# Optimization experiments

Hardware: AMD Instinct MI355X
Metric: run time of the kernel (lower is better)

Reference implementation:

```python
import jax, jax.numpy as jnp
import numpy as np

TOP_K = 2
CAP_FACTOR = 1.25


def _gelu(x):
    # custom tanh GELU matching the torch module
    return 0.5 * x * (1.0 + jnp.tanh(jnp.sqrt(2.0 / jnp.pi) * (x + 0.044715 * x ** 3)))


def setup_inputs() -> dict:
    key = jax.random.key(0)
    ks = jax.random.split(key, 6)
    B, S, D, F, E = 4, 2048, 1024, 4096, 8
    return {
        "hidden_states": jax.random.normal(ks[0], (B, S, D), dtype=jnp.float32),
        "wr": jax.random.normal(ks[1], (E, D), dtype=jnp.float32) * 0.02,  # router weight (Linear, no bias)
        "w1": jax.random.normal(ks[2], (E, D, F), dtype=jnp.float32) * 0.02,
        "b1": jnp.zeros((E, F), dtype=jnp.float32),
        "w2": jax.random.normal(ks[3], (E, F, D), dtype=jnp.float32) * 0.02,
        "b2": jnp.zeros((E, D), dtype=jnp.float32),
    }


def reference(hidden_states, wr, w1, b1, w2, b2):
    B, S, D = hidden_states.shape
    E = wr.shape[0]
    x = hidden_states.reshape(-1, D)  # [T, D]
    T = x.shape[0]

    # ---- router (eval mode: no noise) ----
    logits = x @ wr.T  # [T, E]
    vals, idx = jax.lax.top_k(logits, TOP_K)  # [T, K]
    sparse = jnp.full((T, E), -jnp.inf, dtype=logits.dtype)
    sparse = sparse.at[jnp.arange(T)[:, None], idx].set(vals)
    gating = jax.nn.softmax(sparse, axis=-1)  # [T, E], zero off top-k

    # ---- capacity-limited dispatch ----
    cap = max(8, int(max(1, T * TOP_K // E) * CAP_FACTOR))
    mask = (idx[:, :, None] == jnp.arange(E)).any(axis=1)  # [T, E]
    pos = jnp.cumsum(mask.astype(jnp.int32), axis=0) - 1  # rank of token within expert
    keep = mask & (pos < cap)
    slot = jnp.where(keep, pos, cap)  # overflow -> dummy slot
    e_grid = jnp.broadcast_to(jnp.arange(E)[None, :], (T, E))
    t_grid = jnp.broadcast_to(jnp.arange(T)[:, None], (T, E))
    dispatch = jnp.full((E, cap + 1), T, dtype=jnp.int32)
    dispatch = dispatch.at[e_grid, slot].set(t_grid)[:, :cap]  # [E, cap], T = pad

    # ---- grouped expert MLP ----
    x_pad = jnp.concatenate([x, jnp.zeros((1, D), x.dtype)], axis=0)
    g_pad = jnp.concatenate([gating, jnp.zeros((1, E), gating.dtype)], axis=0)
    xg = x_pad[dispatch]  # [E, cap, D]
    h = _gelu(jnp.einsum('ecd,edf->ecf', xg, w1) + b1[:, None, :])
    y = jnp.einsum('ecf,efd->ecd', h, w2) + b2[:, None, :]  # [E, cap, D]
    g = g_pad[dispatch, jnp.arange(E)[:, None]]  # [E, cap]; 0 for padded slots
    wy = y * g[..., None]

    # ---- combine (scatter-add) ----
    out = jax.ops.segment_sum(wy.reshape(-1, D), dispatch.reshape(-1), num_segments=T + 1)[:T]
    return out.reshape(B, S, D)
```

## Files before the change

kernel.cpp:

```cpp
#include <hip/hip_runtime.h>
#include <cstdint>
#include <cstddef>

#define T_TOK 8192
#define D_DIM 1024
#define F_DIM 4096
#define E_NUM 8
#define CAP   2560
#define BKS   32
#define MYB   20

typedef __attribute__((ext_vector_type(8))) short bf16x8;
typedef __attribute__((ext_vector_type(4))) float f32x4;

typedef const __attribute__((address_space(1))) void* gas_ptr;
typedef __attribute__((address_space(3))) void* las_ptr;

__device__ __forceinline__ unsigned short f2bf(float f) {
  unsigned u = __float_as_uint(f);
  u += 0x7FFF + ((u >> 16) & 1);
  return (unsigned short)(u >> 16);
}

__device__ __forceinline__ float gelu_f(float x) {
  float u = 0.7978845608028654f * (x + 0.044715f * x * x * x);
  float t = 1.0f - 2.0f / (__expf(2.0f * u) + 1.0f);
  return 0.5f * x * (1.0f + t);
}

__device__ __forceinline__ int xcd_swizzle(int bid, int nwg) {
  int q = nwg >> 3;
  return (bid & 7) * q + (bid >> 3);
}

__global__ __launch_bounds__(256) void route_kernel(
    const float* __restrict__ x, const float* __restrict__ wr,
    unsigned short* __restrict__ xbf, int2* __restrict__ tokE,
    float2* __restrict__ tokG)
{
  int tid = threadIdx.x;
  int l = tid & 63;
  int w = tid >> 6;
  int t = blockIdx.x * 4 + w;
  const float4* xr = (const float4*)(x + (size_t)t * D_DIM);
  ushort4* xbr = (ushort4*)(xbf + (size_t)t * D_DIM);
  float acc[E_NUM];
#pragma unroll
  for (int e = 0; e < E_NUM; ++e) acc[e] = 0.f;
#pragma unroll
  for (int c = 0; c < D_DIM / 256; ++c) {
    float4 xv = xr[c * 64 + l];
    ushort4 bv;
    bv.x = f2bf(xv.x); bv.y = f2bf(xv.y); bv.z = f2bf(xv.z); bv.w = f2bf(xv.w);
    xbr[c * 64 + l] = bv;
#pragma unroll
    for (int e = 0; e < E_NUM; ++e) {
      float4 wv = ((const float4*)(wr + (size_t)e * D_DIM))[c * 64 + l];
      acc[e] += xv.x * wv.x + xv.y * wv.y + xv.z * wv.z + xv.w * wv.w;
    }
  }
#pragma unroll
  for (int e = 0; e < E_NUM; ++e) {
#pragma unroll
    for (int s = 32; s > 0; s >>= 1) acc[e] += __shfl_xor(acc[e], s);
  }
  if (l == 0) {
    int e1 = 0; float v1 = acc[0];
#pragma unroll
    for (int e = 1; e < E_NUM; ++e) if (acc[e] > v1) { v1 = acc[e]; e1 = e; }
    int e2 = -1; float v2 = -3.4e38f;
#pragma unroll
    for (int e = 0; e < E_NUM; ++e) if (e != e1 && acc[e] > v2) { v2 = acc[e]; e2 = e; }
    float s = __expf(v2 - v1);
    float g1 = 1.f / (1.f + s);
    tokE[t] = make_int2(e1, e2);
    tokG[t] = make_float2(g1, s * g1);
  }
}

__global__ __launch_bounds__(256) void scan_kernel(
    const int2* __restrict__ tokE, const float2* __restrict__ tokG,
    int* __restrict__ dispatch, float* __restrict__ sgate)
{
  int e = blockIdx.x;
  int tid = threadIdx.x;
  int l = tid & 63;
  int w = tid >> 6;
  __shared__ int wsum[4];
  int base = 0;
  for (int chunk = 0; chunk < T_TOK; chunk += 256) {
    int t = chunk + tid;
    int2 te = tokE[t];
    float2 tg = tokG[t];
    bool f1 = (te.x == e);
    bool f2 = (te.y == e);
    bool f = f1 || f2;
    unsigned long long m = __ballot(f);
    int rank = __popcll(m & ((1ull << l) - 1ull));
    if (l == 0) wsum[w] = __popcll(m);
    __syncthreads();
    int woff = 0;
#pragma unroll
    for (int i = 0; i < 4; ++i) if (i < w) woff += wsum[i];
    int tot = wsum[0] + wsum[1] + wsum[2] + wsum[3];
    int pos = base + woff + rank;
    if (f && pos < CAP) {
      dispatch[e * CAP + pos] = t;
      sgate[e * CAP + pos] = f1 ? tg.x : tg.y;
    }
    base += tot;
    __syncthreads();
  }
  int start = base < CAP ? base : CAP;
  for (int p = start + tid; p < CAP; p += 256) {
    dispatch[e * CAP + p] = T_TOK;
    sgate[e * CAP + p] = 0.f;
  }
}

__global__ __launch_bounds__(256) void transpose_kernel(
    const float* __restrict__ src, unsigned short* __restrict__ dst,
    int K, int N)
{
  const float* s = src + (size_t)blockIdx.z * K * N;
  unsigned short* d = dst + (size_t)blockIdx.z * K * N;
  __shared__ float tile[32][33];
  int tx = threadIdx.x & 31;
  int ty = threadIdx.x >> 5;
  int n0 = blockIdx.x * 32;
  int k0 = blockIdx.y * 32;
#pragma unroll
  for (int i = 0; i < 4; ++i)
    tile[ty + i * 8][tx] = s[(size_t)(k0 + ty + i * 8) * N + n0 + tx];
  __syncthreads();
#pragma unroll
  for (int i = 0; i < 4; ++i)
    d[(size_t)(n0 + ty + i * 8) * K + k0 + tx] = f2bf(tile[tx][ty + i * 8]);
}

#define G1_NXB (F_DIM / 128)
__global__ __launch_bounds__(256, 4) void gemm1_kernel(
    const unsigned short* __restrict__ xbf,
    const unsigned short* __restrict__ w1t,
    const float* __restrict__ b1,
    const int* __restrict__ dispatch,
    unsigned short* __restrict__ h,
    int e_base, size_t w1stride, size_t hstride)
{
  int wg = xcd_swizzle(blockIdx.x, gridDim.x);
  int my = wg % MYB;
  int p  = wg / MYB;
  int nx = p % G1_NXB;
  int ez = p / G1_NXB;
  int e = e_base + ez;
  const unsigned short* w1e = w1t + (size_t)ez * w1stride;
  unsigned short* he = h + (size_t)ez * hstride;
  int n0 = nx * 128;
  int m0 = my * 128;
  int tid = threadIdx.x;
  int l = tid & 63;
  int wid = tid >> 6;
  int wm = wid >> 1, wn = wid & 1;
  int lrow = l & 15, lhi = l >> 4;

  __shared__ __align__(16) unsigned short As[2][128 * BKS];
  __shared__ __align__(16) unsigned short Bs[2][128 * BKS];

  int slot = tid & 3;
  const unsigned short* asrc[2];
  const unsigned short* bsrc[2];
#pragma unroll
  for (int i = 0; i < 2; ++i) {
    int row = i * 64 + (tid >> 2);
    int r = m0 + row;
    int tok = (r < CAP) ? dispatch[e * CAP + r] : T_TOK;
    asrc[i] = xbf + (size_t)tok * D_DIM + slot * 8;
    bsrc[i] = w1e + (size_t)(n0 + row) * D_DIM + slot * 8;
  }

  f32x4 acc[4][4];
#pragma unroll
  for (int m = 0; m < 4; ++m)
#pragma unroll
    for (int n = 0; n < 4; ++n) acc[m][n] = (f32x4){0.f, 0.f, 0.f, 0.f};

  const int NK = D_DIM / BKS;
#pragma unroll
  for (int i = 0; i < 2; ++i) {
    __builtin_amdgcn_global_load_lds((gas_ptr)(asrc[i]),
        (las_ptr)&As[0][(i * 256 + wid * 64) * 8], 16, 0, 0);
    __builtin_amdgcn_global_load_lds((gas_ptr)(bsrc[i]),
        (las_ptr)&Bs[0][(i * 256 + wid * 64) * 8], 16, 0, 0);
  }
  __syncthreads();

  for (int t = 0; t < NK; ++t) {
    int cur = t & 1;
    if (t + 1 < NK) {
      int nxt = cur ^ 1;
      int k0 = (t + 1) * BKS;
#pragma unroll
      for (int i = 0; i < 2; ++i) {
        __builtin_amdgcn_global_load_lds((gas_ptr)(asrc[i] + k0),
            (las_ptr)&As[nxt][(i * 256 + wid * 64) * 8], 16, 0, 0);
        __builtin_amdgcn_global_load_lds((gas_ptr)(bsrc[i] + k0),
            (las_ptr)&Bs[nxt][(i * 256 + wid * 64) * 8], 16, 0, 0);
      }
    }
    bf16x8 af[4], bfr[4];
#pragma unroll
    for (int m = 0; m < 4; ++m) {
      int row = wm * 64 + m * 16 + lrow;
      af[m] = *(const bf16x8*)&As[cur][row * BKS + lhi * 8];
    }
#pragma unroll
    for (int n = 0; n < 4; ++n) {
      int col = wn * 64 + n * 16 + lrow;
      bfr[n] = *(const bf16x8*)&Bs[cur][col * BKS + lhi * 8];
    }
#pragma unroll
    for (int m = 0; m < 4; ++m)
#pragma unroll
      for (int n = 0; n < 4; ++n)
        acc[m][n] = __builtin_amdgcn_mfma_f32_16x16x32_bf16(af[m], bfr[n], acc[m][n], 0, 0, 0);
    __syncthreads();
  }

  int colg[4]; float b1v[4];
#pragma unroll
  for (int n = 0; n < 4; ++n) {
    colg[n] = n0 + wn * 64 + n * 16 + lrow;
    b1v[n] = b1[e * F_DIM + colg[n]];
  }
#pragma unroll
  for (int m = 0; m < 4; ++m) {
    int rb = m0 + wm * 64 + m * 16 + lhi * 4;
#pragma unroll
    for (int j = 0; j < 4; ++j) {
      int r = rb + j;
      if (r < CAP) {
        unsigned short* hr = he + (size_t)r * F_DIM;
#pragma unroll
        for (int n = 0; n < 4; ++n) {
          float v = acc[m][n][j] + b1v[n];
          hr[colg[n]] = f2bf(gelu_f(v));
        }
      }
    }
  }
}

#define G2_NXB (D_DIM / 128)
__global__ __launch_bounds__(256, 4) void gemm2_kernel(
    const unsigned short* __restrict__ h,
    const unsigned short* __restrict__ w2t,
    const float* __restrict__ b2,
    const int* __restrict__ dispatch,
    const float* __restrict__ sgate,
    float* __restrict__ out,
    int e_base, size_t w2stride, size_t hstride)
{
  int wg = xcd_swizzle(blockIdx.x, gridDim.x);
  int my = wg % MYB;
  int p  = wg / MYB;
  int nx = p % G2_NXB;
  int ez = p / G2_NXB;
  int e = e_base + ez;
  const unsigned short* he = h + (size_t)ez * hstride;
  const unsigned short* w2e = w2t + (size_t)ez * w2stride;
  int n0 = nx * 128;
  int m0 = my * 128;
  int tid = threadIdx.x;
  int l = tid & 63;
  int wid = tid >> 6;
  int wm = wid >> 1, wn = wid & 1;
  int lrow = l & 15, lhi = l >> 4;

  __shared__ __align__(16) unsigned short As[2][128 * BKS];
  __shared__ __align__(16) unsigned short Bs[2][128 * BKS];

  int slot = tid & 3;
  const unsigned short* asrc[2];
  const unsigned short* bsrc[2];
#pragma unroll
  for (int i = 0; i < 2; ++i) {
    int row = i * 64 + (tid >> 2);
    int r = m0 + row; if (r >= CAP) r = CAP - 1;
    asrc[i] = he + (size_t)r * F_DIM + slot * 8;
    bsrc[i] = w2e + (size_t)(n0 + row) * F_DIM + slot * 8;
  }

  f32x4 acc[4][4];
#pragma unroll
  for (int m = 0; m < 4; ++m)
#pragma unroll
    for (int n = 0; n < 4; ++n) acc[m][n] = (f32x4){0.f, 0.f, 0.f, 0.f};

  const int NK = F_DIM / BKS;
#pragma unroll
  for (int i = 0; i < 2; ++i) {
    __builtin_amdgcn_global_load_lds((gas_ptr)(asrc[i]),
        (las_ptr)&As[0][(i * 256 + wid * 64) * 8], 16, 0, 0);
    __builtin_amdgcn_global_load_lds((gas_ptr)(bsrc[i]),
        (las_ptr)&Bs[0][(i * 256 + wid * 64) * 8], 16, 0, 0);
  }
  __syncthreads();

  for (int t = 0; t < NK; ++t) {
    int cur = t & 1;
    if (t + 1 < NK) {
      int nxt = cur ^ 1;
      int k0 = (t + 1) * BKS;
#pragma unroll
      for (int i = 0; i < 2; ++i) {
        __builtin_amdgcn_global_load_lds((gas_ptr)(asrc[i] + k0),
            (las_ptr)&As[nxt][(i * 256 + wid * 64) * 8], 16, 0, 0);
        __builtin_amdgcn_global_load_lds((gas_ptr)(bsrc[i] + k0),
            (las_ptr)&Bs[nxt][(i * 256 + wid * 64) * 8], 16, 0, 0);
      }
    }
    bf16x8 af[4], bfr[4];
#pragma unroll
    for (int m = 0; m < 4; ++m) {
      int row = wm * 64 + m * 16 + lrow;
      af[m] = *(const bf16x8*)&As[cur][row * BKS + lhi * 8];
    }
#pragma unroll
    for (int n = 0; n < 4; ++n) {
      int col = wn * 64 + n * 16 + lrow;
      bfr[n] = *(const bf16x8*)&Bs[cur][col * BKS + lhi * 8];
    }
#pragma unroll
    for (int m = 0; m < 4; ++m)
#pragma unroll
      for (int n = 0; n < 4; ++n)
        acc[m][n] = __builtin_amdgcn_mfma_f32_16x16x32_bf16(af[m], bfr[n], acc[m][n], 0, 0, 0);
    __syncthreads();
  }

  int colg[4]; float b2v[4];
#pragma unroll
  for (int n = 0; n < 4; ++n) {
    colg[n] = n0 + wn * 64 + n * 16 + lrow;
    b2v[n] = b2[e * D_DIM + colg[n]];
  }
#pragma unroll
  for (int m = 0; m < 4; ++m) {
    int rb = m0 + wm * 64 + m * 16 + lhi * 4;
#pragma unroll
    for (int j = 0; j < 4; ++j) {
      int r = rb + j;
      if (r < CAP) {
        int tok = dispatch[e * CAP + r];
        if (tok < T_TOK) {
          float g = sgate[e * CAP + r];
          float* orow = out + (size_t)tok * D_DIM;
#pragma unroll
          for (int n = 0; n < 4; ++n)
            atomicAdd(&orow[colg[n]], g * (acc[m][n][j] + b2v[n]));
        }
      }
    }
  }
}

extern "C" void kernel_launch(void* const* d_in, const int* in_sizes, int n_in,
                              void* d_out, int out_size, void* d_ws, size_t ws_size,
                              hipStream_t stream) {
  const float* x  = (const float*)d_in[0];
  const float* wr = (const float*)d_in[1];
  const float* w1 = (const float*)d_in[2];
  const float* b1 = (const float*)d_in[3];
  const float* w2 = (const float*)d_in[4];
  const float* b2 = (const float*)d_in[5];
  float* out = (float*)d_out;

  char* ws = (char*)d_ws;
  size_t off = 0;
  auto alloc = [&](size_t bytes) -> void* {
    off = (off + 255) & ~(size_t)255;
    void* p = ws + off;
    off += bytes;
    return p;
  };
  int*   dispatch = (int*)alloc((size_t)E_NUM * CAP * 4);
  float* sgate    = (float*)alloc((size_t)E_NUM * CAP * 4);
  int2*  tokE     = (int2*)alloc((size_t)T_TOK * 8);
  float2* tokG    = (float2*)alloc((size_t)T_TOK * 8);
  unsigned short* xbf = (unsigned short*)alloc((size_t)(T_TOK + 1) * D_DIM * 2);

  const size_t wsz = (size_t)D_DIM * F_DIM * 2;
  const size_t hsz = (size_t)CAP * F_DIM * 2;
  size_t remain = ws_size > off ? ws_size - off : 0;
  bool tierA = remain >= (size_t)E_NUM * (2 * wsz + hsz) + (size_t)(1 << 16);

  hipMemsetAsync(out, 0, (size_t)T_TOK * D_DIM * 4, stream);
  hipMemsetAsync(xbf + (size_t)T_TOK * D_DIM, 0, D_DIM * 2, stream);
  route_kernel<<<T_TOK / 4, 256, 0, stream>>>(x, wr, xbf, tokE, tokG);
  scan_kernel<<<E_NUM, 256, 0, stream>>>(tokE, tokG, dispatch, sgate);

  if (tierA) {
    unsigned short* w1t = (unsigned short*)alloc((size_t)E_NUM * wsz);
    unsigned short* w2t = (unsigned short*)alloc((size_t)E_NUM * wsz);
    unsigned short* hb  = (unsigned short*)alloc((size_t)E_NUM * hsz);
    transpose_kernel<<<dim3(F_DIM / 32, D_DIM / 32, E_NUM), 256, 0, stream>>>(w1, w1t, D_DIM, F_DIM);
    transpose_kernel<<<dim3(D_DIM / 32, F_DIM / 32, E_NUM), 256, 0, stream>>>(w2, w2t, F_DIM, D_DIM);
    gemm1_kernel<<<dim3(G1_NXB * MYB * E_NUM), 256, 0, stream>>>(
        xbf, w1t, b1, dispatch, hb, 0, wsz / 2, hsz / 2);
    gemm2_kernel<<<dim3(G2_NXB * MYB * E_NUM), 256, 0, stream>>>(
        hb, w2t, b2, dispatch, sgate, out, 0, wsz / 2, hsz / 2);
  } else {
    unsigned short* w1t = (unsigned short*)alloc(wsz);
    unsigned short* w2t = (unsigned short*)alloc(wsz);
    unsigned short* hb  = (unsigned short*)alloc(hsz);
    for (int e = 0; e < E_NUM; ++e) {
      transpose_kernel<<<dim3(F_DIM / 32, D_DIM / 32, 1), 256, 0, stream>>>(
          w1 + (size_t)e * D_DIM * F_DIM, w1t, D_DIM, F_DIM);
      gemm1_kernel<<<dim3(G1_NXB * MYB), 256, 0, stream>>>(
          xbf, w1t, b1, dispatch, hb, e, 0, 0);
      transpose_kernel<<<dim3(D_DIM / 32, F_DIM / 32, 1), 256, 0, stream>>>(
          w2 + (size_t)e * D_DIM * F_DIM, w2t, F_DIM, D_DIM);
      gemm2_kernel<<<dim3(G2_NXB * MYB), 256, 0, stream>>>(
          hb, w2t, b2, dispatch, sgate, out, e, 0, 0);
    }
  }
}
```

Measured before the change: 874.0 us.

## Triple-buffer swizzled GEMM pipeline, skip empty expert tiles, vectorize weight transpose

Both expert GEMMs move from a double-buffered loop with full __syncthreads to a three-stage LDS ring. It waits with vmcnt-based barriers, uses XOR-swizzled LDS layouts to avoid bank conflicts, and raises MFMA priority. The scan kernel now records per-expert token counts, so GEMM blocks whose row tile lies beyond an expert's filled capacity exit early. The weight transpose uses 64x64 tiles with float4 loads and 16-byte bf16 stores. The added LDS per block lowers the occupancy hint from 4 to 3 blocks per CU, and early exit depends on routing balance.

```diff
diff --git a/kernel.cpp b/kernel.cpp
--- a/kernel.cpp
+++ b/kernel.cpp
@@ -9,8 +9,10 @@
 #define CAP   2560
 #define BKS   32
 #define MYB   20
+#define LDSB  16384
 
 typedef __attribute__((ext_vector_type(8))) short bf16x8;
+typedef __attribute__((ext_vector_type(8))) unsigned short u16x8;
 typedef __attribute__((ext_vector_type(4))) float f32x4;
 
 typedef const __attribute__((address_space(1))) void* gas_ptr;
@@ -32,6 +34,9 @@
   int q = nwg >> 3;
   return (bid & 7) * q + (bid >> 3);
 }
+
+#define PIPE_BAR4() asm volatile("s_waitcnt vmcnt(4)\n\ts_barrier" ::: "memory")
+#define PIPE_BAR0() asm volatile("s_waitcnt vmcnt(0)\n\ts_barrier" ::: "memory")
 
 __global__ __launch_bounds__(256) void route_kernel(
     const float* __restrict__ x, const float* __restrict__ wr,
@@ -80,7 +85,7 @@
 
 __global__ __launch_bounds__(256) void scan_kernel(
     const int2* __restrict__ tokE, const float2* __restrict__ tokG,
-    int* __restrict__ dispatch, float* __restrict__ sgate)
+    int* __restrict__ dispatch, float* __restrict__ sgate, int* __restrict__ cnt)
 {
   int e = blockIdx.x;
   int tid = threadIdx.x;
@@ -116,6 +121,7 @@
     dispatch[e * CAP + p] = T_TOK;
     sgate[e * CAP + p] = 0.f;
   }
+  if (tid == 0) cnt[e] = base < CAP ? base : CAP;
 }
 
 __global__ __launch_bounds__(256) void transpose_kernel(
@@ -124,26 +130,40 @@
 {
   const float* s = src + (size_t)blockIdx.z * K * N;
   unsigned short* d = dst + (size_t)blockIdx.z * K * N;
-  __shared__ float tile[32][33];
-  int tx = threadIdx.x & 31;
-  int ty = threadIdx.x >> 5;
-  int n0 = blockIdx.x * 32;
-  int k0 = blockIdx.y * 32;
-#pragma unroll
-  for (int i = 0; i < 4; ++i)
-    tile[ty + i * 8][tx] = s[(size_t)(k0 + ty + i * 8) * N + n0 + tx];
+  __shared__ float tile[64][65];
+  int n0 = blockIdx.x * 64;
+  int k0 = blockIdx.y * 64;
+  int tid = threadIdx.x;
+  int r = tid >> 4;
+  int c4 = (tid & 15) * 4;
+#pragma unroll
+  for (int i = 0; i < 4; ++i) {
+    int row = r + i * 16;
+    float4 v = *(const float4*)&s[(size_t)(k0 + row) * N + n0 + c4];
+    tile[row][c4] = v.x; tile[row][c4 + 1] = v.y;
+    tile[row][c4 + 2] = v.z; tile[row][c4 + 3] = v.w;
+  }
   __syncthreads();
-#pragma unroll
-  for (int i = 0; i < 4; ++i)
-    d[(size_t)(n0 + ty + i * 8) * K + k0 + tx] = f2bf(tile[tx][ty + i * 8]);
-}
+  int n = tid >> 2;
+  int kg = tid & 3;
+#pragma unroll
+  for (int j = 0; j < 2; ++j) {
+    int kc = kg * 2 + j;
+    u16x8 o;
+#pragma unroll
+    for (int q = 0; q < 8; ++q) o[q] = f2bf(tile[kc * 8 + q][n]);
+    *(u16x8*)&d[(size_t)(n0 + n) * K + k0 + kc * 8] = o;
+  }
+}
+
 
 #define G1_NXB (F_DIM / 128)
-__global__ __launch_bounds__(256, 4) void gemm1_kernel(
+__global__ __launch_bounds__(256, 3) void gemm1_kernel(
     const unsigned short* __restrict__ xbf,
     const unsigned short* __restrict__ w1t,
     const float* __restrict__ b1,
     const int* __restrict__ dispatch,
+    const int* __restrict__ cnt,
     unsigned short* __restrict__ h,
     int e_base, size_t w1stride, size_t hstride)
 {
@@ -153,29 +173,44 @@
   int nx = p % G1_NXB;
   int ez = p / G1_NXB;
   int e = e_base + ez;
+  int m0 = my * 128;
+  if (m0 >= cnt[e]) return;
   const unsigned short* w1e = w1t + (size_t)ez * w1stride;
   unsigned short* he = h + (size_t)ez * hstride;
   int n0 = nx * 128;
-  int m0 = my * 128;
   int tid = threadIdx.x;
   int l = tid & 63;
   int wid = tid >> 6;
   int wm = wid >> 1, wn = wid & 1;
   int lrow = l & 15, lhi = l >> 4;
 
-  __shared__ __align__(16) unsigned short As[2][128 * BKS];
-  __shared__ __align__(16) unsigned short Bs[2][128 * BKS];
-
-  int slot = tid & 3;
-  const unsigned short* asrc[2];
-  const unsigned short* bsrc[2];
-#pragma unroll
-  for (int i = 0; i < 2; ++i) {
-    int row = i * 64 + (tid >> 2);
-    int r = m0 + row;
-    int tok = (r < CAP) ? dispatch[e * CAP + r] : T_TOK;
-    asrc[i] = xbf + (size_t)tok * D_DIM + slot * 8;
-    bsrc[i] = w1e + (size_t)(n0 + row) * D_DIM + slot * 8;
+  __shared__ __align__(16) char lds[3 * LDSB];
+
+  const unsigned short* ag[2];
+  const unsigned short* bg[2];
+  int ldsA[2], ldsB[2];
+#pragma unroll
+  for (int j = 0; j < 2; ++j) {
+    int chunk = wid * 2 + j;
+    int U = chunk * 64 + l;
+    int u = U ^ ((U >> 3) & 7);
+    int row = u >> 2, s = u & 3;
+    int tok = dispatch[e * CAP + m0 + row];
+    ag[j] = xbf + (size_t)tok * D_DIM + s * 8;
+    bg[j] = w1e + (size_t)(n0 + row) * D_DIM + s * 8;
+    ldsA[j] = chunk * 1024;
+    ldsB[j] = 8192 + chunk * 1024;
+  }
+
+  int aoff[4], boff[4];
+#pragma unroll
+  for (int m = 0; m < 4; ++m) {
+    int row = wm * 64 + m * 16 + lrow;
+    int u = row * 4 + lhi;
+    aoff[m] = (u ^ ((row >> 1) & 7)) * 16;
+    int colr = wn * 64 + m * 16 + lrow;
+    int ub = colr * 4 + lhi;
+    boff[m] = 8192 + (ub ^ ((colr >> 1) & 7)) * 16;
   }
 
   f32x4 acc[4][4];
@@ -184,46 +219,38 @@
 #pragma unroll
     for (int n = 0; n < 4; ++n) acc[m][n] = (f32x4){0.f, 0.f, 0.f, 0.f};
 
-  const int NK = D_DIM / BKS;
-#pragma unroll
-  for (int i = 0; i < 2; ++i) {
-    __builtin_amdgcn_global_load_lds((gas_ptr)(asrc[i]),
-        (las_ptr)&As[0][(i * 256 + wid * 64) * 8], 16, 0, 0);
-    __builtin_amdgcn_global_load_lds((gas_ptr)(bsrc[i]),
-        (las_ptr)&Bs[0][(i * 256 + wid * 64) * 8], 16, 0, 0);
-  }
-  __syncthreads();
-
-  for (int t = 0; t < NK; ++t) {
-    int cur = t & 1;
-    if (t + 1 < NK) {
-      int nxt = cur ^ 1;
-      int k0 = (t + 1) * BKS;
-#pragma unroll
-      for (int i = 0; i < 2; ++i) {
-        __builtin_amdgcn_global_load_lds((gas_ptr)(asrc[i] + k0),
-            (las_ptr)&As[nxt][(i * 256 + wid * 64) * 8], 16, 0, 0);
-        __builtin_amdgcn_global_load_lds((gas_ptr)(bsrc[i] + k0),
-            (las_ptr)&Bs[nxt][(i * 256 + wid * 64) * 8], 16, 0, 0);
-      }
-    }
+#define STAGE1(BASE, KOFF) do { \
+    __builtin_amdgcn_global_load_lds((gas_ptr)(ag[0] + (KOFF)), (las_ptr)(lds + (BASE) + ldsA[0]), 16, 0, 0); \
+    __builtin_amdgcn_global_load_lds((gas_ptr)(bg[0] + (KOFF)), (las_ptr)(lds + (BASE) + ldsB[0]), 16, 0, 0); \
+    __builtin_amdgcn_global_load_lds((gas_ptr)(ag[1] + (KOFF)), (las_ptr)(lds + (BASE) + ldsA[1]), 16, 0, 0); \
+    __builtin_amdgcn_global_load_lds((gas_ptr)(bg[1] + (KOFF)), (las_ptr)(lds + (BASE) + ldsB[1]), 16, 0, 0); \
+  } while (0)
+
+  const int NT = D_DIM / BKS;
+  STAGE1(0, 0);
+  STAGE1(LDSB, BKS);
+  PIPE_BAR4();
+
+  int cb = 0, sb = 2 * LDSB, koff = 2 * BKS;
+  for (int t = 0; t < NT; ++t) {
+    if (t + 2 < NT) { STAGE1(sb, koff); koff += BKS; }
     bf16x8 af[4], bfr[4];
 #pragma unroll
-    for (int m = 0; m < 4; ++m) {
-      int row = wm * 64 + m * 16 + lrow;
-      af[m] = *(const bf16x8*)&As[cur][row * BKS + lhi * 8];
-    }
-#pragma unroll
-    for (int n = 0; n < 4; ++n) {
-      int col = wn * 64 + n * 16 + lrow;
-      bfr[n] = *(const bf16x8*)&Bs[cur][col * BKS + lhi * 8];
-    }
+    for (int m = 0; m < 4; ++m) af[m] = *(const bf16x8*)(lds + cb + aoff[m]);
+#pragma unroll
+    for (int n = 0; n < 4; ++n) bfr[n] = *(const bf16x8*)(lds + cb + boff[n]);
+    __builtin_amdgcn_s_setprio(1);
 #pragma unroll
     for (int m = 0; m < 4; ++m)
 #pragma unroll
       for (int n = 0; n < 4; ++n)
         acc[m][n] = __builtin_amdgcn_mfma_f32_16x16x32_bf16(af[m], bfr[n], acc[m][n], 0, 0, 0);
-    __syncthreads();
+    __builtin_amdgcn_s_setprio(0);
+    if (t + 1 < NT) {
+      if (t + 2 < NT) PIPE_BAR4(); else PIPE_BAR0();
+      cb = (cb == 2 * LDSB) ? 0 : cb + LDSB;
+      sb = (sb == 2 * LDSB) ? 0 : sb + LDSB;
+    }
   }
 
   int colg[4]; float b1v[4];
@@ -238,25 +265,24 @@
 #pragma unroll
     for (int j = 0; j < 4; ++j) {
       int r = rb + j;
-      if (r < CAP) {
-        unsigned short* hr = he + (size_t)r * F_DIM;
-#pragma unroll
-        for (int n = 0; n < 4; ++n) {
-          float v = acc[m][n][j] + b1v[n];
-          hr[colg[n]] = f2bf(gelu_f(v));
-        }
+      unsigned short* hr = he + (size_t)r * F_DIM;
+#pragma unroll
+      for (int n = 0; n < 4; ++n) {
+        float v = acc[m][n][j] + b1v[n];
+        hr[colg[n]] = f2bf(gelu_f(v));
       }
     }
   }
 }
 
 #define G2_NXB (D_DIM / 128)
-__global__ __launch_bounds__(256, 4) void gemm2_kernel(
+__global__ __launch_bounds__(256, 3) void gemm2_kernel(
     const unsigned short* __restrict__ h,
     const unsigned short* __restrict__ w2t,
     const float* __restrict__ b2,
     const int* __restrict__ dispatch,
     const float* __restrict__ sgate,
+    const int* __restrict__ cnt,
     float* __restrict__ out,
     int e_base, size_t w2stride, size_t hstride)
 {
@@ -266,28 +292,43 @@
   int nx = p % G2_NXB;
   int ez = p / G2_NXB;
   int e = e_base + ez;
+  int m0 = my * 128;
+  if (m0 >= cnt[e]) return;
   const unsigned short* he = h + (size_t)ez * hstride;
   const unsigned short* w2e = w2t + (size_t)ez * w2stride;
   int n0 = nx * 128;
-  int m0 = my * 128;
   int tid = threadIdx.x;
   int l = tid & 63;
   int wid = tid >> 6;
   int wm = wid >> 1, wn = wid & 1;
   int lrow = l & 15, lhi = l >> 4;
 
-  __shared__ __align__(16) unsigned short As[2][128 * BKS];
-  __shared__ __align__(16) unsigned short Bs[2][128 * BKS];
-
-  int slot = tid & 3;
-  const unsigned short* asrc[2];
-  const unsigned short* bsrc[2];
-#pragma unroll
-  for (int i = 0; i < 2; ++i) {
-    int row = i * 64 + (tid >> 2);
-    int r = m0 + row; if (r >= CAP) r = CAP - 1;
-    asrc[i] = he + (size_t)r * F_DIM + slot * 8;
-    bsrc[i] = w2e + (size_t)(n0 + row) * F_DIM + slot * 8;
+  __shared__ __align__(16) char lds[3 * LDSB];
+
+  const unsigned short* ag[2];
+  const unsigned short* bg[2];
+  int ldsA[2], ldsB[2];
+#pragma unroll
+  for (int j = 0; j < 2; ++j) {
+    int chunk = wid * 2 + j;
+    int U = chunk * 64 + l;
+    int u = U ^ ((U >> 3) & 7);
+    int row = u >> 2, s = u & 3;
+    ag[j] = he + (size_t)(m0 + row) * F_DIM + s * 8;
+    bg[j] = w2e + (size_t)(n0 + row) * F_DIM + s * 8;
+    ldsA[j] = chunk * 1024;
+    ldsB[j] = 8192 + chunk * 1024;
+  }
+
+  int aoff[4], boff[4];
+#pragma unroll
+  for (int m = 0; m < 4; ++m) {
+    int row = wm * 64 + m * 16 + lrow;
+    int u = row * 4 + lhi;
+    aoff[m] = (u ^ ((row >> 1) & 7)) * 16;
+    int colr = wn * 64 + m * 16 + lrow;
+    int ub = colr * 4 + lhi;
+    boff[m] = 8192 + (ub ^ ((colr >> 1) & 7)) * 16;
   }
 
   f32x4 acc[4][4];
@@ -296,46 +337,38 @@
 #pragma unroll
     for (int n = 0; n < 4; ++n) acc[m][n] = (f32x4){0.f, 0.f, 0.f, 0.f};
 
-  const int NK = F_DIM / BKS;
-#pragma unroll
-  for (int i = 0; i < 2; ++i) {
-    __builtin_amdgcn_global_load_lds((gas_ptr)(asrc[i]),
-        (las_ptr)&As[0][(i * 256 + wid * 64) * 8], 16, 0, 0);
-    __builtin_amdgcn_global_load_lds((gas_ptr)(bsrc[i]),
-        (las_ptr)&Bs[0][(i * 256 + wid * 64) * 8], 16, 0, 0);
-  }
-  __syncthreads();
-
-  for (int t = 0; t < NK; ++t) {
-    int cur = t & 1;
-    if (t + 1 < NK) {
-      int nxt = cur ^ 1;
-      int k0 = (t + 1) * BKS;
-#pragma unroll
-      for (int i = 0; i < 2; ++i) {
-        __builtin_amdgcn_global_load_lds((gas_ptr)(asrc[i] + k0),
-            (las_ptr)&As[nxt][(i * 256 + wid * 64) * 8], 16, 0, 0);
-        __builtin_amdgcn_global_load_lds((gas_ptr)(bsrc[i] + k0),
-            (las_ptr)&Bs[nxt][(i * 256 + wid * 64) * 8], 16, 0, 0);
-      }
-    }
+#define STAGE2(BASE, KOFF) do { \
+    __builtin_amdgcn_global_load_lds((gas_ptr)(ag[0] + (KOFF)), (las_ptr)(lds + (BASE) + ldsA[0]), 16, 0, 0); \
+    __builtin_amdgcn_global_load_lds((gas_ptr)(bg[0] + (KOFF)), (las_ptr)(lds + (BASE) + ldsB[0]), 16, 0, 0); \
+    __builtin_amdgcn_global_load_lds((gas_ptr)(ag[1] + (KOFF)), (las_ptr)(lds + (BASE) + ldsA[1]), 16, 0, 0); \
+    __builtin_amdgcn_global_load_lds((gas_ptr)(bg[1] + (KOFF)), (las_ptr)(lds + (BASE) + ldsB[1]), 16, 0, 0); \
+  } while (0)
+
+  const int NT = F_DIM / BKS;
+  STAGE2(0, 0);
+  STAGE2(LDSB, BKS);
+  PIPE_BAR4();
+
+  int cb = 0, sb = 2 * LDSB, koff = 2 * BKS;
+  for (int t = 0; t < NT; ++t) {
+    if (t + 2 < NT) { STAGE2(sb, koff); koff += BKS; }
     bf16x8 af[4], bfr[4];
 #pragma unroll
-    for (int m = 0; m < 4; ++m) {
-      int row = wm * 64 + m * 16 + lrow;
-      af[m] = *(const bf16x8*)&As[cur][row * BKS + lhi * 8];
-    }
-#pragma unroll
-    for (int n = 0; n < 4; ++n) {
-      int col = wn * 64 + n * 16 + lrow;
-      bfr[n] = *(const bf16x8*)&Bs[cur][col * BKS + lhi * 8];
-    }
+    for (int m = 0; m < 4; ++m) af[m] = *(const bf16x8*)(lds + cb + aoff[m]);
+#pragma unroll
+    for (int n = 0; n < 4; ++n) bfr[n] = *(const bf16x8*)(lds + cb + boff[n]);
+    __builtin_amdgcn_s_setprio(1);
 #pragma unroll
     for (int m = 0; m < 4; ++m)
 #pragma unroll
       for (int n = 0; n < 4; ++n)
         acc[m][n] = __builtin_amdgcn_mfma_f32_16x16x32_bf16(af[m], bfr[n], acc[m][n], 0, 0, 0);
-    __syncthreads();
+    __builtin_amdgcn_s_setprio(0);
+    if (t + 1 < NT) {
+      if (t + 2 < NT) PIPE_BAR4(); else PIPE_BAR0();
+      cb = (cb == 2 * LDSB) ? 0 : cb + LDSB;
+      sb = (sb == 2 * LDSB) ? 0 : sb + LDSB;
+    }
   }
 
   int colg[4]; float b2v[4];
@@ -350,15 +383,13 @@
 #pragma unroll
     for (int j = 0; j < 4; ++j) {
       int r = rb + j;
-      if (r < CAP) {
-        int tok = dispatch[e * CAP + r];
-        if (tok < T_TOK) {
-          float g = sgate[e * CAP + r];
-          float* orow = out + (size_t)tok * D_DIM;
-#pragma unroll
-          for (int n = 0; n < 4; ++n)
-            atomicAdd(&orow[colg[n]], g * (acc[m][n][j] + b2v[n]));
-        }
+      int tok = dispatch[e * CAP + r];
+      if (tok < T_TOK) {
+        float g = sgate[e * CAP + r];
+        float* orow = out + (size_t)tok * D_DIM;
+#pragma unroll
+        for (int n = 0; n < 4; ++n)
+          atomicAdd(&orow[colg[n]], g * (acc[m][n][j] + b2v[n]));
       }
     }
   }
@@ -385,6 +416,7 @@
   };
   int*   dispatch = (int*)alloc((size_t)E_NUM * CAP * 4);
   float* sgate    = (float*)alloc((size_t)E_NUM * CAP * 4);
+  int*   cnt      = (int*)alloc((size_t)E_NUM * 4);
   int2*  tokE     = (int2*)alloc((size_t)T_TOK * 8);
   float2* tokG    = (float2*)alloc((size_t)T_TOK * 8);
   unsigned short* xbf = (unsigned short*)alloc((size_t)(T_TOK + 1) * D_DIM * 2);
@@ -397,31 +429,31 @@
   hipMemsetAsync(out, 0, (size_t)T_TOK * D_DIM * 4, stream);
   hipMemsetAsync(xbf + (size_t)T_TOK * D_DIM, 0, D_DIM * 2, stream);
   route_kernel<<<T_TOK / 4, 256, 0, stream>>>(x, wr, xbf, tokE, tokG);
-  scan_kernel<<<E_NUM, 256, 0, stream>>>(tokE, tokG, dispatch, sgate);
+  scan_kernel<<<E_NUM, 256, 0, stream>>>(tokE, tokG, dispatch, sgate, cnt);
 
   if (tierA) {
     unsigned short* w1t = (unsigned short*)alloc((size_t)E_NUM * wsz);
     unsigned short* w2t = (unsigned short*)alloc((size_t)E_NUM * wsz);
     unsigned short* hb  = (unsigned short*)alloc((size_t)E_NUM * hsz);
-    transpose_kernel<<<dim3(F_DIM / 32, D_DIM / 32, E_NUM), 256, 0, stream>>>(w1, w1t, D_DIM, F_DIM);
-    transpose_kernel<<<dim3(D_DIM / 32, F_DIM / 32, E_NUM), 256, 0, stream>>>(w2, w2t, F_DIM, D_DIM);
+    transpose_kernel<<<dim3(F_DIM / 64, D_DIM / 64, E_NUM), 256, 0, stream>>>(w1, w1t, D_DIM, F_DIM);
+    transpose_kernel<<<dim3(D_DIM / 64, F_DIM / 64, E_NUM), 256, 0, stream>>>(w2, w2t, F_DIM, D_DIM);
     gemm1_kernel<<<dim3(G1_NXB * MYB * E_NUM), 256, 0, stream>>>(
-        xbf, w1t, b1, dispatch, hb, 0, wsz / 2, hsz / 2);
+        xbf, w1t, b1, dispatch, cnt, hb, 0, wsz / 2, hsz / 2);
     gemm2_kernel<<<dim3(G2_NXB * MYB * E_NUM), 256, 0, stream>>>(
-        hb, w2t, b2, dispatch, sgate, out, 0, wsz / 2, hsz / 2);
+        hb, w2t, b2, dispatch, sgate, cnt, out, 0, wsz / 2, hsz / 2);
   } else {
     unsigned short* w1t = (unsigned short*)alloc(wsz);
     unsigned short* w2t = (unsigned short*)alloc(wsz);
     unsigned short* hb  = (unsigned short*)alloc(hsz);
     for (int e = 0; e < E_NUM; ++e) {
-      transpose_kernel<<<dim3(F_DIM / 32, D_DIM / 32, 1), 256, 0, stream>>>(
+      transpose_kernel<<<dim3(F_DIM / 64, D_DIM / 64, 1), 256, 0, stream>>>(
           w1 + (size_t)e * D_DIM * F_DIM, w1t, D_DIM, F_DIM);
       gemm1_kernel<<<dim3(G1_NXB * MYB), 256, 0, stream>>>(
-          xbf, w1t, b1, dispatch, hb, e, 0, 0);
-      transpose_kernel<<<dim3(D_DIM / 32, F_DIM / 32, 1), 256, 0, stream>>>(
+          xbf, w1t, b1, dispatch, cnt, hb, e, 0, 0);
+      transpose_kernel<<<dim3(D_DIM / 64, F_DIM / 64, 1), 256, 0, stream>>>(
           w2 + (size_t)e * D_DIM * F_DIM, w2t, F_DIM, D_DIM);
       gemm2_kernel<<<dim3(G2_NXB * MYB), 256, 0, stream>>>(
-          hb, w2t, b2, dispatch, sgate, out, e, 0, 0);
-    }
-  }
-}
+          hb, w2t, b2, dispatch, sgate, cnt, out, e, 0, 0);
+    }
+  }
+}
```

New measurement: 774.0 us. 11.4% less time.
